# Kernel optimization log

Measured on AMD Instinct MI355X. Metric: run time of the kernel, lower is better.

The kernel has to match this reference:

```python
import jax, jax.numpy as jnp
import numpy as np

INPDIM = 512
RECDIM = 512


def setup_inputs() -> dict:
    key = jax.random.key(0)
    k1, k2, k3, k4 = jax.random.split(key, 4)
    x = jax.random.normal(k1, (64, 1024, INPDIM), dtype=jnp.float32)
    W = jax.random.normal(k2, (INPDIM, RECDIM), dtype=jnp.float32) / np.sqrt(INPDIM)
    # per-unit recurrent weight vector, kept in (-1, 1) for stability
    u = jax.random.uniform(k3, (RECDIM,), dtype=jnp.float32, minval=-1.0, maxval=1.0)
    b = jax.random.normal(k4, (RECDIM,), dtype=jnp.float32) * 0.01
    return {"x": x, "W": W, "u": u, "b": b}


def reference(x, W, u, b):
    # IndRNN: h_t = relu(x_t @ W + u * h_{t-1} + b), h_0 = ones(recdim)
    B, T, _ = x.shape
    # Batch the input projection as one big GEMM (time-independent part).
    xp = jnp.einsum('bti,ir->btr', x, W) + b  # [B, T, R]
    h0 = jnp.ones((B, W.shape[1]), dtype=x.dtype)

    def step(h, xp_t):
        h = jax.nn.relu(xp_t + u * h)
        return h, h

    _, hs = jax.lax.scan(step, h0, jnp.swapaxes(xp, 0, 1))  # hs: [T, B, R]
    return jnp.swapaxes(hs, 0, 1)  # [B, T, R]
```

## Files before the change

kernel.cpp:

```cpp
#include <hip/hip_runtime.h>
#include <stdint.h>

typedef __attribute__((ext_vector_type(8))) short short8;
typedef __attribute__((ext_vector_type(8))) unsigned short ushort8;
typedef __attribute__((ext_vector_type(4))) float f32x4;

#define LDST 40
#define XPST 66

static __device__ __forceinline__ unsigned short f2bf(float f) {
    union { float f; uint32_t u; } v; v.f = f;
    uint32_t u = v.u;
    u += 0x7fffu + ((u >> 16) & 1u);
    return (unsigned short)(u >> 16);
}

__global__ __launch_bounds__(256)
void wt_kernel(const float* __restrict__ W, unsigned short* __restrict__ Wt)
{
    __shared__ float s[32][33];
    const int tx = threadIdx.x;
    const int ty = threadIdx.y;
    const int kBase = blockIdx.x * 32;
    const int nBase = blockIdx.y * 32;
    #pragma unroll
    for (int j = 0; j < 4; ++j)
        s[ty + 8 * j][tx] = W[(size_t)(kBase + ty + 8 * j) * 512 + nBase + tx];
    __syncthreads();
    #pragma unroll
    for (int j = 0; j < 4; ++j)
        Wt[(size_t)(nBase + ty + 8 * j) * 512 + kBase + tx] = f2bf(s[tx][ty + 8 * j]);
}

__global__ __launch_bounds__(256, 2)
void fused_kernel(const float* __restrict__ X, const unsigned short* __restrict__ Wt,
                  const float* __restrict__ bias, const float* __restrict__ u,
                  float* __restrict__ out)
{
    __shared__ unsigned short As[2][128 * LDST];
    __shared__ unsigned short Bs[2][64 * LDST];
    __shared__ float xpL[128 * XPST];

    const int tid = threadIdx.x;
    const int bx  = blockIdx.x;
    const int b   = bx & 63;
    const int rb  = bx >> 6;

    const int lane  = tid & 63;
    const int wave  = tid >> 6;
    const int m16   = lane & 15;
    const int quad  = lane >> 4;
    const int waveM = wave & 1;
    const int waveN = wave >> 1;

    const int aRow8 = tid >> 3;
    const int aK    = (tid & 7) * 4;
    const int bRow  = tid >> 2;
    const int bK    = (tid & 3) * 8;

    const float ur = u[rb * 64 + (tid & 63)];
    const float br = bias[rb * 64 + (tid & 63)];
    float h = 1.0f;

    f32x4 acc[4][2] = {};
    float4 aF[4];
    ushort8 bF;

    const float* xB = X + (size_t)b * 1024 * 512;
    const unsigned short* wB = Wt + (size_t)(rb * 64) * 512;

    #pragma unroll
    for (int p = 0; p < 4; ++p)
        aF[p] = *(const float4*)(xB + (size_t)(p * 32 + aRow8) * 512 + aK);
    bF = *(const ushort8*)(wB + (size_t)bRow * 512 + bK);

    for (int tt = 0; tt < 8; ++tt) {
        for (int ki = 0; ki < 16; ++ki) {
            const int buf = ki & 1;
            #pragma unroll
            for (int p = 0; p < 4; ++p) {
                ushort4 us;
                us.x = f2bf(aF[p].x); us.y = f2bf(aF[p].y);
                us.z = f2bf(aF[p].z); us.w = f2bf(aF[p].w);
                *(ushort4*)&As[buf][(p * 32 + aRow8) * LDST + aK] = us;
            }
            *(ushort8*)&Bs[buf][bRow * LDST + bK] = bF;
            __syncthreads();

            int nki = ki + 1, ntt = tt;
            if (nki == 16) { nki = 0; ++ntt; }
            if (ntt < 8) {
                const float* xT = xB + (size_t)(ntt * 128) * 512 + (size_t)nki * 32;
                #pragma unroll
                for (int p = 0; p < 4; ++p)
                    aF[p] = *(const float4*)(xT + (size_t)(p * 32 + aRow8) * 512 + aK);
                bF = *(const ushort8*)(wB + (size_t)bRow * 512 + (size_t)nki * 32 + bK);
            }

            short8 af[4], bf2[2];
            #pragma unroll
            for (int mi = 0; mi < 4; ++mi)
                af[mi] = *(const short8*)&As[buf][(waveM * 64 + mi * 16 + m16) * LDST + quad * 8];
            #pragma unroll
            for (int ni = 0; ni < 2; ++ni)
                bf2[ni] = *(const short8*)&Bs[buf][(waveN * 32 + ni * 16 + m16) * LDST + quad * 8];
            #pragma unroll
            for (int mi = 0; mi < 4; ++mi)
                #pragma unroll
                for (int ni = 0; ni < 2; ++ni)
                    acc[mi][ni] = __builtin_amdgcn_mfma_f32_16x16x32_bf16(
                        af[mi], bf2[ni], acc[mi][ni], 0, 0, 0);
            __syncthreads();
        }

        #pragma unroll
        for (int mi = 0; mi < 4; ++mi) {
            const int t0 = waveM * 64 + mi * 16 + quad * 4;
            #pragma unroll
            for (int ni = 0; ni < 2; ++ni) {
                const int r = waveN * 32 + ni * 16 + m16;
                #pragma unroll
                for (int rr = 0; rr < 4; ++rr)
                    xpL[(t0 + rr) * XPST + r] = acc[mi][ni][rr];
                acc[mi][ni] = (f32x4){0.f, 0.f, 0.f, 0.f};
            }
        }
        __syncthreads();

        if (tid < 64) {
            float* o = out + ((size_t)b * 1024 + (size_t)tt * 128) * 512 + rb * 64 + tid;
            for (int t0 = 0; t0 < 128; t0 += 16) {
                float v[16];
                #pragma unroll
                for (int j = 0; j < 16; ++j) v[j] = xpL[(t0 + j) * XPST + tid] + br;
                #pragma unroll
                for (int j = 0; j < 16; ++j) {
                    h = fmaxf(fmaf(ur, h, v[j]), 0.0f);
                    o[(size_t)(t0 + j) * 512] = h;
                }
            }
        }
    }
}

extern "C" void kernel_launch(void* const* d_in, const int* in_sizes, int n_in,
                              void* d_out, int out_size, void* d_ws, size_t ws_size,
                              hipStream_t stream) {
    const float* x = (const float*)d_in[0];
    const float* W = (const float*)d_in[1];
    const float* u = (const float*)d_in[2];
    const float* b = (const float*)d_in[3];
    float* out = (float*)d_out;

    unsigned short* Wt = (unsigned short*)d_ws;

    dim3 tgrid(16, 16), tblk(32, 8);
    wt_kernel<<<tgrid, tblk, 0, stream>>>(W, Wt);
    fused_kernel<<<512, 256, 0, stream>>>(x, Wt, b, u, out);
}
```

Baseline: 338.7 us.

## Keep full W slice resident in swizzled LDS and stream X directly to MFMA registers

The fused kernel now loads the block's whole 64x512 bf16 weight slice into LDS once, with an XOR swizzle against bank conflicts. X is read straight from global memory into MFMA operand registers with a cheaper round-to-nearest bf16 pack, so the per-k-step LDS staging and the two barriers per step are gone. The xp staging buffer is stored as fp16 to fit within 80KB of dynamic LDS. Risks: lower occupancy from the larger LDS footprint, less coalesced direct X loads, an extra precision loss from fp16 xp, and no prefetch pipelining of X.

```diff
diff --git a/kernel.cpp b/kernel.cpp
--- a/kernel.cpp
+++ b/kernel.cpp
@@ -1,12 +1,10 @@
 #include <hip/hip_runtime.h>
+#include <hip/hip_fp16.h>
 #include <stdint.h>
 
 typedef __attribute__((ext_vector_type(8))) short short8;
 typedef __attribute__((ext_vector_type(8))) unsigned short ushort8;
 typedef __attribute__((ext_vector_type(4))) float f32x4;
-
-#define LDST 40
-#define XPST 66
 
 static __device__ __forceinline__ unsigned short f2bf(float f) {
     union { float f; uint32_t u; } v; v.f = f;
@@ -14,6 +12,14 @@
     u += 0x7fffu + ((u >> 16) & 1u);
     return (unsigned short)(u >> 16);
 }
+
+static __device__ __forceinline__ uint32_t pk_bf16(float a, float b) {
+    union { float f; uint32_t u; } ua, ub;
+    ua.f = a; ub.f = b;
+    return ((ua.u + 0x8000u) >> 16) | ((ub.u + 0x8000u) & 0xffff0000u);
+}
+
+#define BSW(n, g) ((g) ^ ((n) & 7))
 
 __global__ __launch_bounds__(256)
 void wt_kernel(const float* __restrict__ W, unsigned short* __restrict__ Wt)
@@ -37,9 +43,9 @@
                   const float* __restrict__ bias, const float* __restrict__ u,
                   float* __restrict__ out)
 {
-    __shared__ unsigned short As[2][128 * LDST];
-    __shared__ unsigned short Bs[2][64 * LDST];
-    __shared__ float xpL[128 * XPST];
+    extern __shared__ unsigned char smem[];
+    unsigned short* Bs = (unsigned short*)smem;
+    __half*         xpL = (__half*)(smem + 65536);
 
     const int tid = threadIdx.x;
     const int bx  = blockIdx.x;
@@ -53,65 +59,65 @@
     const int waveM = wave & 1;
     const int waveN = wave >> 1;
 
-    const int aRow8 = tid >> 3;
-    const int aK    = (tid & 7) * 4;
-    const int bRow  = tid >> 2;
-    const int bK    = (tid & 3) * 8;
+    {
+        const int w = wave, p = lane;
+        #pragma unroll
+        for (int it = 0; it < 16; ++it) {
+            const int n = it * 4 + w;
+            const int g = BSW(n, p);
+            ushort8 v = *(const ushort8*)(Wt + (size_t)(rb * 64 + n) * 512 + g * 8);
+            *(ushort8*)(Bs + n * 512 + p * 8) = v;
+        }
+    }
+    __syncthreads();
 
-    const float ur = u[rb * 64 + (tid & 63)];
-    const float br = bias[rb * 64 + (tid & 63)];
+    const float ur = u[rb * 64 + lane];
+    const float br = bias[rb * 64 + lane];
     float h = 1.0f;
 
-    f32x4 acc[4][2] = {};
-    float4 aF[4];
-    ushort8 bF;
-
     const float* xB = X + (size_t)b * 1024 * 512;
-    const unsigned short* wB = Wt + (size_t)(rb * 64) * 512;
-
-    #pragma unroll
-    for (int p = 0; p < 4; ++p)
-        aF[p] = *(const float4*)(xB + (size_t)(p * 32 + aRow8) * 512 + aK);
-    bF = *(const ushort8*)(wB + (size_t)bRow * 512 + bK);
+    f32x4 acc[4][2];
 
     for (int tt = 0; tt < 8; ++tt) {
-        for (int ki = 0; ki < 16; ++ki) {
-            const int buf = ki & 1;
-            #pragma unroll
-            for (int p = 0; p < 4; ++p) {
-                ushort4 us;
-                us.x = f2bf(aF[p].x); us.y = f2bf(aF[p].y);
-                us.z = f2bf(aF[p].z); us.w = f2bf(aF[p].w);
-                *(ushort4*)&As[buf][(p * 32 + aRow8) * LDST + aK] = us;
-            }
-            *(ushort8*)&Bs[buf][bRow * LDST + bK] = bF;
-            __syncthreads();
-
-            int nki = ki + 1, ntt = tt;
-            if (nki == 16) { nki = 0; ++ntt; }
-            if (ntt < 8) {
-                const float* xT = xB + (size_t)(ntt * 128) * 512 + (size_t)nki * 32;
-                #pragma unroll
-                for (int p = 0; p < 4; ++p)
-                    aF[p] = *(const float4*)(xT + (size_t)(p * 32 + aRow8) * 512 + aK);
-                bF = *(const ushort8*)(wB + (size_t)bRow * 512 + (size_t)nki * 32 + bK);
-            }
-
-            short8 af[4], bf2[2];
-            #pragma unroll
-            for (int mi = 0; mi < 4; ++mi)
-                af[mi] = *(const short8*)&As[buf][(waveM * 64 + mi * 16 + m16) * LDST + quad * 8];
+        #pragma unroll
+        for (int mi = 0; mi < 4; ++mi)
             #pragma unroll
             for (int ni = 0; ni < 2; ++ni)
-                bf2[ni] = *(const short8*)&Bs[buf][(waveN * 32 + ni * 16 + m16) * LDST + quad * 8];
+                acc[mi][ni] = (f32x4){0.f, 0.f, 0.f, 0.f};
+
+        #pragma unroll 2
+        for (int kk = 0; kk < 16; ++kk) {
+            const int k0 = kk * 32 + quad * 8;
+            short8 af[4];
+            #pragma unroll
+            for (int mi = 0; mi < 4; ++mi) {
+                const int m = tt * 128 + waveM * 64 + mi * 16 + m16;
+                const float* s = xB + (size_t)m * 512 + k0;
+                float4 v0 = *(const float4*)(s);
+                float4 v1 = *(const float4*)(s + 4);
+                union { uint32_t u[4]; short8 s8; } cv;
+                cv.u[0] = pk_bf16(v0.x, v0.y);
+                cv.u[1] = pk_bf16(v0.z, v0.w);
+                cv.u[2] = pk_bf16(v1.x, v1.y);
+                cv.u[3] = pk_bf16(v1.z, v1.w);
+                af[mi] = cv.s8;
+            }
+            short8 bf[2];
+            #pragma unroll
+            for (int ni = 0; ni < 2; ++ni) {
+                const int n = waveN * 32 + ni * 16 + m16;
+                const int p = BSW(n, kk * 4 + quad);
+                bf[ni] = *(const short8*)(Bs + n * 512 + p * 8);
+            }
             #pragma unroll
             for (int mi = 0; mi < 4; ++mi)
                 #pragma unroll
                 for (int ni = 0; ni < 2; ++ni)
                     acc[mi][ni] = __builtin_amdgcn_mfma_f32_16x16x32_bf16(
-                        af[mi], bf2[ni], acc[mi][ni], 0, 0, 0);
-            __syncthreads();
+                        af[mi], bf[ni], acc[mi][ni], 0, 0, 0);
         }
+
+        __syncthreads();
 
         #pragma unroll
         for (int mi = 0; mi < 4; ++mi) {
@@ -121,18 +127,18 @@
                 const int r = waveN * 32 + ni * 16 + m16;
                 #pragma unroll
                 for (int rr = 0; rr < 4; ++rr)
-                    xpL[(t0 + rr) * XPST + r] = acc[mi][ni][rr];
-                acc[mi][ni] = (f32x4){0.f, 0.f, 0.f, 0.f};
+                    xpL[(t0 + rr) * 64 + r] = __float2half(acc[mi][ni][rr]);
             }
         }
         __syncthreads();
 
-        if (tid < 64) {
-            float* o = out + ((size_t)b * 1024 + (size_t)tt * 128) * 512 + rb * 64 + tid;
+        if (wave == 0) {
+            float* o = out + ((size_t)b * 1024 + (size_t)tt * 128) * 512 + rb * 64 + lane;
             for (int t0 = 0; t0 < 128; t0 += 16) {
                 float v[16];
                 #pragma unroll
-                for (int j = 0; j < 16; ++j) v[j] = xpL[(t0 + j) * XPST + tid] + br;
+                for (int j = 0; j < 16; ++j)
+                    v[j] = __half2float(xpL[(t0 + j) * 64 + lane]) + br;
                 #pragma unroll
                 for (int j = 0; j < 16; ++j) {
                     h = fmaxf(fmaf(ur, h, v[j]), 0.0f);
@@ -156,5 +162,9 @@
 
     dim3 tgrid(16, 16), tblk(32, 8);
     wt_kernel<<<tgrid, tblk, 0, stream>>>(W, Wt);
-    fused_kernel<<<512, 256, 0, stream>>>(x, Wt, b, u, out);
+
+    const int lds_bytes = 65536 + 16384;
+    hipFuncSetAttribute((const void*)fused_kernel,
+                        hipFuncAttributeMaxDynamicSharedMemorySize, lds_bytes);
+    fused_kernel<<<512, 256, lds_bytes, stream>>>(x, Wt, b, u, out);
 }
```

After: 433.1 us. +27.9%, slower.
